# Performance work log

Measured on AMD Instinct MI355X. Metric: run time of the kernel, lower is better.

Reference implementation:

```python
import jax, jax.numpy as jnp
import numpy as np

B, N, E = 2, 50000, 400000
C_IN, D, C, S, H, L, FFN = 5, 2, 128, 32, 8, 4, 512
COORD_F, TIME_F, FREQ_BASE, BETA = 8, 4, 1000.0, 1.0
HD = C // H


def setup_inputs() -> dict:
    key = jax.random.key(0)
    ks = jax.random.split(key, 32)
    sc = 0.02
    inp = {
        'inputs': jax.random.normal(ks[0], (B, N, C_IN), jnp.float32),
        'coords': jax.random.uniform(ks[1], (B, N, D), jnp.float32),
        't_norm': jax.random.uniform(ks[2], (B,), jnp.float32),
        'adj_indices': jax.random.randint(ks[3], (2, E), 0, N, jnp.int64 if jax.config.jax_enable_x64 else jnp.int32),
        'adj_values': jax.random.uniform(ks[4], (E,), jnp.float32) * 0.25,  # ~1/avg_degree for stable magnitudes
        'freq_matrix': jax.random.normal(ks[5], (D, COORD_F), jnp.float32),
        'embed_W': jax.random.normal(ks[6], (C_IN + 2 * COORD_F + 2 * TIME_F, C), jnp.float32) * sc,
        'embed_b': jnp.zeros((C,), jnp.float32),
        'ln1_g': jnp.ones((L, C), jnp.float32),
        'ln1_b': jnp.zeros((L, C), jnp.float32),
        'Wslice': jax.random.normal(ks[7], (L, C, S), jnp.float32) * sc,
        'bslice': jnp.zeros((L, S), jnp.float32),
        'Wfront': jax.random.normal(ks[8], (L, C, S), jnp.float32) * sc,
        'bfront': jnp.zeros((L, S), jnp.float32),
        'Win': jax.random.normal(ks[9], (L, C, 3 * C), jnp.float32) * sc,
        'b_in': jnp.zeros((L, 3 * C), jnp.float32),
        'Wout': jax.random.normal(ks[10], (L, C, C), jnp.float32) * sc,
        'bout': jnp.zeros((L, C), jnp.float32),
        'ln2_g': jnp.ones((L, C), jnp.float32),
        'ln2_b': jnp.zeros((L, C), jnp.float32),
        'Wff1': jax.random.normal(ks[11], (L, C, FFN), jnp.float32) * sc,
        'bff1': jnp.zeros((L, FFN), jnp.float32),
        'Wff2': jax.random.normal(ks[12], (L, FFN, C), jnp.float32) * sc,
        'bff2': jnp.zeros((L, C), jnp.float32),
        'proj_W': jax.random.normal(ks[13], (C, C_IN), jnp.float32) * sc,
        'proj_b': jnp.zeros((C_IN,), jnp.float32),
    }
    return inp


def _layer_norm(x, g, b, eps=1e-5):
    m = jnp.mean(x, -1, keepdims=True)
    v = jnp.mean(jnp.square(x - m), -1, keepdims=True)
    return (x - m) * jax.lax.rsqrt(v + eps) * g + b


def _forward(inputs, coords, t_norm, adj_indices, adj_values, freq_matrix,
             embed_W, embed_b, ln1_g, ln1_b, Wslice, bslice, Wfront, bfront,
             Win, b_in, Wout, bout, ln2_g, ln2_b, Wff1, bff1, Wff2, bff2,
             proj_W, proj_b):
    rows, cols = adj_indices[0], adj_indices[1]
    b, n = coords.shape[0], coords.shape[1]
    # spatial Fourier encoding (B,N,2*COORD_F)
    p = 2.0 * jnp.pi * (coords @ freq_matrix)
    sp_enc = jnp.concatenate([jnp.sin(p), jnp.cos(p)], -1)
    # temporal encoding (B,N,2*TIME_F)
    omega = FREQ_BASE ** (-jnp.arange(TIME_F, dtype=jnp.float32) / TIME_F)
    ang = omega[None, :] * (t_norm * FREQ_BASE)[:, None]
    t_enc = jnp.broadcast_to(jnp.concatenate([jnp.sin(ang), jnp.cos(ang)], -1)[:, None, :], (b, n, 2 * TIME_F))
    x = jnp.concatenate([inputs, sp_enc, t_enc], -1) @ embed_W + embed_b  # (B,N,C)
    weights_all = []
    for l in range(L):
        h = _layer_norm(x, ln1_g[l], ln1_b[l])
        # sparse adjacency aggregation: y[r] += a_e * h[c] (duplicates sum == coalesce)
        contrib = adj_values[None, :, None] * h[:, cols, :]  # (B,E,C)
        h_local = jax.vmap(lambda cb: jax.ops.segment_sum(cb, rows, num_segments=n))(contrib)
        h_front = h - h_local
        logits = h @ Wslice[l] + bslice[l] + BETA * (h_front @ Wfront[l] + bfront[l])
        w = jax.nn.softmax(logits, -1)  # (B,N,S)
        wsum = jnp.maximum(jnp.sum(w, axis=1)[:, :, None], 1e-8)  # (B,S,1)
        slices = jnp.einsum('bns,bnc->bsc', w, h) / wsum  # (B,S,C)
        # slice-space MHA (self-attention on S tokens)
        qkv = slices @ Win[l] + b_in[l]
        q, k, v = jnp.split(qkv, 3, axis=-1)
        def split_heads(t):
            return t.reshape(b, S, H, HD).transpose(0, 2, 1, 3)  # (B,H,S,HD)
        qh, kh, vh = split_heads(q), split_heads(k), split_heads(v)
        attn = jax.nn.softmax(jnp.einsum('bhqd,bhkd->bhqk', qh, kh) / jnp.sqrt(jnp.float32(HD)), -1)
        o = jnp.einsum('bhqk,bhkd->bhqd', attn, vh).transpose(0, 2, 1, 3).reshape(b, S, C)
        slices_out = o @ Wout[l] + bout[l]
        x = x + jnp.einsum('bns,bsc->bnc', w, slices_out)
        h2 = _layer_norm(x, ln2_g[l], ln2_b[l])
        x = x + jax.nn.gelu(h2 @ Wff1[l] + bff1[l], approximate=False) @ Wff2[l] + bff2[l]
        weights_all.append(w)
    out = x @ proj_W + proj_b  # (B,N,C_OUT)
    return out, jnp.stack(weights_all)  # (L,B,N,S)


def reference(inputs, coords, t_norm, adj_indices, adj_values, freq_matrix,
              embed_W, embed_b, ln1_g, ln1_b, Wslice, bslice, Wfront, bfront,
              Win, b_in, Wout, bout, ln2_g, ln2_b, Wff1, bff1, Wff2, bff2,
              proj_W, proj_b):
    return _forward(inputs, coords, t_norm, adj_indices, adj_values, freq_matrix,
                    embed_W, embed_b, ln1_g, ln1_b, Wslice, bslice, Wfront, bfront,
                    Win, b_in, Wout, bout, ln2_g, ln2_b, Wff1, bff1, Wff2, bff2,
                    proj_W, proj_b)
```

## Files before the change

kernel.cpp:

```cpp
#include <hip/hip_runtime.h>
#include <math.h>

#define BATCH 2
#define NN 50000
#define NE 400000
#define C_IN 5
#define CC 128
#define SS 32
#define NH 8
#define NL 4
#define FFN 512
#define COORD_F 8
#define TIME_F 4
#define HD 16
#define BETA 1.0f
#define TWO_PI 6.283185307179586476925287f

#define NTOT (BATCH * NN)
#define FF_MT 128
#define FF_BLOCKS ((NTOT + FF_MT - 1) / FF_MT)
#define MPAD (FF_BLOCKS * FF_MT)
#define NBLK ((NN + 127) / 128)
#define LP_PAD 136
#define H2S 136
#define HIDS 72
#define NREP 16
#define EMB_NPB 8
#define PROJ_NPB 12

typedef unsigned short u16;
typedef unsigned int u32;
typedef __attribute__((ext_vector_type(8))) __bf16 bf16x8;
typedef __attribute__((ext_vector_type(4))) float f32x4;

__device__ __forceinline__ u16 f2bf(float f) {
    union { __bf16 b; u16 u; } v;
    v.b = (__bf16)f;
    return v.u;
}

__device__ __forceinline__ float bf2f(u16 h) {
    union { u32 u; float f; } v; v.u = ((u32)h) << 16;
    return v.f;
}

__device__ __forceinline__ float bf_lo(u32 u) {
    union { u32 u; float f; } v; v.u = u << 16;
    return v.f;
}

__device__ __forceinline__ float bf_hi(u32 u) {
    union { u32 u; float f; } v; v.u = u & 0xffff0000u;
    return v.f;
}

__device__ __forceinline__ float gelu_f(float a) {
    float xx = a * 0.7071067811865475f;
    float ax = fabsf(xx);
    float t = 1.0f / fmaf(0.3275911f, ax, 1.0f);
    float poly = t * fmaf(t, fmaf(t, fmaf(t, fmaf(t, 1.061405429f, -1.453152027f),
                                          1.421413741f), -0.284496736f), 0.254829592f);
    float e = __expf(-ax * ax);
    float erfv = copysignf(fmaf(-poly, e, 1.0f), xx);
    return 0.5f * a * (1.0f + erfv);
}

__global__ void count_deg(const int* rows, int* deg) {
    int e = blockIdx.x * blockDim.x + threadIdx.x;
    if (e < NE) atomicAdd(&deg[rows[e]], 1);
}

__global__ __launch_bounds__(512) void scan_deg(const int* deg, int* rowptr) {
    __shared__ int part[512];
    int t = threadIdx.x;
    const int CH = (NN + 511) / 512;
    int begin = t * CH, end = min(begin + CH, NN);
    int s = 0;
    for (int i = begin; i < end; i++) s += deg[i];
    part[t] = s;
    __syncthreads();
    for (int off = 1; off < 512; off <<= 1) {
        int v = (t >= off) ? part[t - off] : 0;
        __syncthreads();
        part[t] += v;
        __syncthreads();
    }
    int base = (t == 0) ? 0 : part[t - 1];
    for (int i = begin; i < end; i++) { rowptr[i] = base; base += deg[i]; }
    if (t == 511) rowptr[NN] = part[511];
}

__global__ void fill_csr(const int* rows, const int* cols, const float* vals,
                         int* cursor, int* csr_col, float* csr_val) {
    int e = blockIdx.x * blockDim.x + threadIdx.x;
    if (e < NE) {
        int p = atomicAdd(&cursor[rows[e]], 1);
        csr_col[p] = cols[e];
        csr_val[p] = vals[e];
    }
}

__global__ __launch_bounds__(128) void embed_ln1_kernel(const float* __restrict__ inputs,
                                                        const float* __restrict__ coords,
                                                        const float* __restrict__ t_norm,
                                                        const float* __restrict__ freq,
                                                        const float* __restrict__ W,
                                                        const float* __restrict__ bias,
                                                        const float* __restrict__ g,
                                                        const float* __restrict__ bb,
                                                        float* __restrict__ x,
                                                        u16* __restrict__ hbf) {
    int t = threadIdx.x;
    int n0 = blockIdx.x * EMB_NPB;
    __shared__ float feat[EMB_NPB][32];
    __shared__ float sm[EMB_NPB][4];
    if (t < EMB_NPB) {
        int node = n0 + t;
        if (node < NTOT) {
            int b = node / NN;
            float c0 = coords[node * 2 + 0], c1 = coords[node * 2 + 1];
            #pragma unroll
            for (int j = 0; j < 8; j++) {
                float p = TWO_PI * (c0 * freq[j] + c1 * freq[8 + j]);
                feat[t][5 + j] = sinf(p);
                feat[t][13 + j] = cosf(p);
            }
            #pragma unroll
            for (int j = 0; j < 4; j++) {
                float omega = powf(1000.0f, -(float)j * 0.25f);
                float ang = omega * t_norm[b] * 1000.0f;
                feat[t][21 + j] = sinf(ang);
                feat[t][25 + j] = cosf(ang);
            }
            #pragma unroll
            for (int k = 0; k < 5; k++) feat[t][k] = inputs[node * 5 + k];
        }
    }
    float Wr[29];
    #pragma unroll
    for (int k = 0; k < 29; k++) Wr[k] = W[k * CC + t];
    float bi = bias[t], gt = g[t], bbt = bb[t];
    __syncthreads();
    float accv[EMB_NPB];
    #pragma unroll
    for (int nn = 0; nn < EMB_NPB; nn++) {
        float a = bi;
        #pragma unroll
        for (int k = 0; k < 29; k++) a += feat[nn][k] * Wr[k];
        accv[nn] = a;
        int node = n0 + nn;
        if (node < NTOT) x[(size_t)node * CC + t] = a;
    }
    #pragma unroll
    for (int nn = 0; nn < EMB_NPB; nn++) {
        float s = accv[nn];
        #pragma unroll
        for (int off = 32; off > 0; off >>= 1) s += __shfl_xor(s, off, 64);
        if ((t & 63) == 0) sm[nn][t >> 6] = s;
    }
    __syncthreads();
    float dv[EMB_NPB];
    #pragma unroll
    for (int nn = 0; nn < EMB_NPB; nn++) {
        float mean = (sm[nn][0] + sm[nn][1]) * (1.0f / 128.0f);
        float d = accv[nn] - mean;
        dv[nn] = d;
        float ss = d * d;
        #pragma unroll
        for (int off = 32; off > 0; off >>= 1) ss += __shfl_xor(ss, off, 64);
        if ((t & 63) == 0) sm[nn][2 + (t >> 6)] = ss;
    }
    __syncthreads();
    #pragma unroll
    for (int nn = 0; nn < EMB_NPB; nn++) {
        int node = n0 + nn;
        if (node < NTOT) {
            float var = (sm[nn][2] + sm[nn][3]) * (1.0f / 128.0f);
            hbf[(size_t)node * CC + t] = f2bf(dv[nn] * rsqrtf(var + 1e-5f) * gt + bbt);
        }
    }
}

__global__ __launch_bounds__(256) void agg_kernel(const u16* __restrict__ hbf,
                                                  const int* __restrict__ rowptr,
                                                  const int* __restrict__ csr_col,
                                                  const float* __restrict__ csr_val,
                                                  u16* __restrict__ hlbf) {
    int wid = threadIdx.x >> 6;
    int lane = threadIdx.x & 63;
    int node = blockIdx.x * 4 + wid;
    int b = node / NN, r = node - b * NN;
    int s0 = rowptr[r], s1 = rowptr[r + 1];
    const u32* hb = (const u32*)(hbf + (size_t)b * NN * CC);
    float a0l = 0.f, a1l = 0.f, a2l = 0.f, a3l = 0.f;
    float a0h = 0.f, a1h = 0.f, a2h = 0.f, a3h = 0.f;
    int e = s0;
    for (; e + 4 <= s1; e += 4) {
        int c0 = csr_col[e], c1 = csr_col[e + 1], c2 = csr_col[e + 2], c3 = csr_col[e + 3];
        float v0 = csr_val[e], v1 = csr_val[e + 1], v2 = csr_val[e + 2], v3 = csr_val[e + 3];
        u32 u0 = hb[(size_t)c0 * 64 + lane];
        u32 u1 = hb[(size_t)c1 * 64 + lane];
        u32 u2 = hb[(size_t)c2 * 64 + lane];
        u32 u3 = hb[(size_t)c3 * 64 + lane];
        a0l += v0 * bf_lo(u0);  a0h += v0 * bf_hi(u0);
        a1l += v1 * bf_lo(u1);  a1h += v1 * bf_hi(u1);
        a2l += v2 * bf_lo(u2);  a2h += v2 * bf_hi(u2);
        a3l += v3 * bf_lo(u3);  a3h += v3 * bf_hi(u3);
    }
    for (; e < s1; e++) {
        float v = csr_val[e];
        u32 u = hb[(size_t)csr_col[e] * 64 + lane];
        a0l += v * bf_lo(u);  a0h += v * bf_hi(u);
    }
    float al = (a0l + a1l) + (a2l + a3l);
    float ah = (a0h + a1h) + (a2h + a3h);
    u32 outv = (u32)f2bf(al) | ((u32)f2bf(ah) << 16);
    ((u32*)hlbf)[(size_t)node * 64 + lane] = outv;
}

__global__ __launch_bounds__(256) void pack_logits_weights(const float* Ws, const float* bs,
                                                           const float* Wf, const float* bf,
                                                           u16* Wcombp, float* bcombp) {
    int idx = blockIdx.x * 256 + threadIdx.x;
    if (idx >= NL * SS * 256) return;
    int l = idx / (SS * 256);
    int r = idx - l * (SS * 256);
    int s = r >> 8, k = r & 255;
    float v;
    if (k < 128)
        v = Ws[(size_t)l * CC * SS + (size_t)k * SS + s] + BETA * Wf[(size_t)l * CC * SS + (size_t)k * SS + s];
    else
        v = -BETA * Wf[(size_t)l * CC * SS + (size_t)(k - 128) * SS + s];
    Wcombp[idx] = f2bf(v);
    if (k == 0) bcombp[l * SS + s] = bs[l * SS + s] + BETA * bf[l * SS + s];
}

__global__ __launch_bounds__(256, 2) void logits_pool(const u16* __restrict__ hbf,
                                                      const u16* __restrict__ hlbf,
                                                      const u16* __restrict__ Wcomb,
                                                      const float* __restrict__ bcomb,
                                                      float* __restrict__ wout,
                                                      u16* __restrict__ whi,
                                                      u16* __restrict__ wlo,
                                                      float* __restrict__ rep,
                                                      float* __restrict__ wsum) {
    __shared__ __align__(16) u16 hT[128 * LP_PAD];
    __shared__ __align__(16) u16 wTh[SS * LP_PAD];
    __shared__ __align__(16) u16 wTl[SS * LP_PAD];
    __shared__ float wsum_sh[SS];
    int t = threadIdx.x;
    int b = blockIdx.y;
    int nl0 = blockIdx.x * 128;
    int wv = t >> 6, lane = t & 63;
    int q = lane >> 4, ln16 = lane & 15;
    int nl0w = nl0 + wv * 32;
    if (t < SS) wsum_sh[t] = 0.0f;
    __syncthreads();

    f32x4 acc[2][2];
    #pragma unroll
    for (int mi = 0; mi < 2; mi++)
        #pragma unroll
        for (int ni = 0; ni < 2; ni++) acc[mi][ni] = (f32x4){0.f, 0.f, 0.f, 0.f};

    #pragma unroll
    for (int ks = 0; ks < 8; ks++) {
        const u16* src = (ks < 4) ? hbf : hlbf;
        int ko = (ks & 3) * 32 + q * 8;
        bf16x8 af[2], bfrg[2];
        #pragma unroll
        for (int mi = 0; mi < 2; mi++) {
            int nl = nl0w + mi * 16 + ln16;
            af[mi] = *(const bf16x8*)&src[((size_t)b * NN + nl) * CC + ko];
            if (ks < 4) {
                bool valid = nl < NN;
                const u16* ap = (const u16*)&af[mi];
                int nlb = nl - nl0;
                #pragma unroll
                for (int i = 0; i < 8; i++)
                    hT[(ko + i) * LP_PAD + nlb] = valid ? ap[i] : (u16)0;
            }
        }
        #pragma unroll
        for (int ni = 0; ni < 2; ni++)
            bfrg[ni] = *(const bf16x8*)&Wcomb[(size_t)(ni * 16 + ln16) * 256 + ks * 32 + q * 8];
        #pragma unroll
        for (int mi = 0; mi < 2; mi++)
            #pragma unroll
            for (int ni = 0; ni < 2; ni++)
                acc[mi][ni] = __builtin_amdgcn_mfma_f32_16x16x32_bf16(af[mi], bfrg[ni], acc[mi][ni], 0, 0, 0);
    }

    float bc0 = bcomb[ln16], bc1 = bcomb[16 + ln16];
    float ws0 = 0.0f, ws1 = 0.0f;
    #pragma unroll
    for (int mi = 0; mi < 2; mi++)
        #pragma unroll
        for (int r = 0; r < 4; r++) {
            float l0 = acc[mi][0][r] + bc0;
            float l1 = acc[mi][1][r] + bc1;
            float m = fmaxf(l0, l1);
            #pragma unroll
            for (int msk = 1; msk < 16; msk <<= 1) m = fmaxf(m, __shfl_xor(m, msk, 64));
            float e0 = __expf(l0 - m), e1 = __expf(l1 - m);
            float sum = e0 + e1;
            #pragma unroll
            for (int msk = 1; msk < 16; msk <<= 1) sum += __shfl_xor(sum, msk, 64);
            float is = 1.0f / sum;
            int nl = nl0w + mi * 16 + q * 4 + r;
            bool valid = nl < NN;
            float w0 = valid ? e0 * is : 0.0f;
            float w1 = valid ? e1 * is : 0.0f;
            u16 h0 = f2bf(w0), h1 = f2bf(w1);
            u16 lo0 = f2bf(w0 - bf2f(h0)), lo1 = f2bf(w1 - bf2f(h1));
            if (valid) {
                size_t gb = ((size_t)b * NN + nl) * SS;
                wout[gb + ln16] = w0;
                wout[gb + 16 + ln16] = w1;
                whi[gb + ln16] = h0;  wlo[gb + ln16] = lo0;
                whi[gb + 16 + ln16] = h1;  wlo[gb + 16 + ln16] = lo1;
            }
            int nlb = nl - nl0;
            wTh[ln16 * LP_PAD + nlb] = h0;  wTl[ln16 * LP_PAD + nlb] = lo0;
            wTh[(16 + ln16) * LP_PAD + nlb] = h1;  wTl[(16 + ln16) * LP_PAD + nlb] = lo1;
            ws0 += w0;  ws1 += w1;
        }
    ws0 += __shfl_xor(ws0, 16, 64); ws0 += __shfl_xor(ws0, 32, 64);
    ws1 += __shfl_xor(ws1, 16, 64); ws1 += __shfl_xor(ws1, 32, 64);
    if (q == 0) {
        atomicAdd(&wsum_sh[ln16], ws0);
        atomicAdd(&wsum_sh[16 + ln16], ws1);
    }
    __syncthreads();

    f32x4 pacc[2][8];
    #pragma unroll
    for (int st = 0; st < 2; st++)
        #pragma unroll
        for (int ct = 0; ct < 8; ct++) pacc[st][ct] = (f32x4){0.f, 0.f, 0.f, 0.f};
    {
        int kb = wv * 32 + q * 8;
        bf16x8 wh[2], wl2[2];
        #pragma unroll
        for (int st = 0; st < 2; st++) {
            wh[st] = *(const bf16x8*)&wTh[(st * 16 + ln16) * LP_PAD + kb];
            wl2[st] = *(const bf16x8*)&wTl[(st * 16 + ln16) * LP_PAD + kb];
        }
        #pragma unroll
        for (int ct = 0; ct < 8; ct++) {
            bf16x8 bfr = *(const bf16x8*)&hT[(ct * 16 + ln16) * LP_PAD + kb];
            #pragma unroll
            for (int st = 0; st < 2; st++) {
                pacc[st][ct] = __builtin_amdgcn_mfma_f32_16x16x32_bf16(wh[st], bfr, pacc[st][ct], 0, 0, 0);
                pacc[st][ct] = __builtin_amdgcn_mfma_f32_16x16x32_bf16(wl2[st], bfr, pacc[st][ct], 0, 0, 0);
            }
        }
    }
    __syncthreads();

    float* red = (float*)hT;
    for (int i = t; i < SS * CC; i += 256) red[i] = 0.0f;
    __syncthreads();
    #pragma unroll
    for (int st = 0; st < 2; st++)
        #pragma unroll
        for (int ct = 0; ct < 8; ct++)
            #pragma unroll
            for (int r = 0; r < 4; r++)
                atomicAdd(&red[(st * 16 + q * 4 + r) * CC + ct * 16 + ln16], pacc[st][ct][r]);
    __syncthreads();
    if (t < SS) atomicAdd(&wsum[b * SS + t], wsum_sh[t]);
    int rep_id = (blockIdx.y * NBLK + blockIdx.x) & (NREP - 1);
    float* dst = rep + ((size_t)rep_id * BATCH + b) * SS * CC;
    #pragma unroll
    for (int k = 0; k < 16; k++) {
        int idx = k * 256 + t;
        atomicAdd(&dst[idx], red[idx]);
    }
}

__global__ __launch_bounds__(256) void reduce_slices(const float* __restrict__ rep,
                                                     float* __restrict__ slices_acc) {
    int j = blockIdx.x * 256 + threadIdx.x;
    int b = j >> 12;
    int e = j & 4095;
    float s = 0.0f;
    #pragma unroll
    for (int r = 0; r < NREP; r++) s += rep[((size_t)r * BATCH + b) * SS * CC + e];
    slices_acc[(size_t)b * SS * CC + e] = s;
}

__global__ __launch_bounds__(128) void qkv_kernel(const float* slices_acc, const float* wsum,
                                                  const float* Win, const float* b_in_p,
                                                  float* qkv) {
    int blk = blockIdx.x;
    int t = threadIdx.x;
    __shared__ float row[128];
    float iv = 1.0f / fmaxf(wsum[blk], 1e-8f);
    row[t] = slices_acc[(size_t)blk * CC + t] * iv;
    __syncthreads();
    #pragma unroll
    for (int jj = 0; jj < 3; jj++) {
        int j = t + jj * 128;
        float a = b_in_p[j];
        #pragma unroll 8
        for (int c = 0; c < 128; c++) a += row[c] * Win[c * 384 + j];
        qkv[(size_t)blk * 384 + j] = a;
    }
}

__global__ __launch_bounds__(64) void attn_kernel(const float* qkv, float* ovals) {
    int blk = blockIdx.x;
    int b = blk >> 3, h = blk & 7;
    int t = threadIdx.x;
    __shared__ float ksh[32 * 16], vsh[32 * 16];
    for (int i = t; i < 512; i += 64) {
        int k = i >> 4, d = i & 15;
        ksh[i] = qkv[((size_t)b * 32 + k) * 384 + 128 + h * 16 + d];
        vsh[i] = qkv[((size_t)b * 32 + k) * 384 + 256 + h * 16 + d];
    }
    __syncthreads();
    if (t < 32) {
        float qr[16];
        #pragma unroll
        for (int d = 0; d < 16; d++) qr[d] = qkv[((size_t)b * 32 + t) * 384 + h * 16 + d];
        float sc[32];
        float m = -1e30f;
        for (int k = 0; k < 32; k++) {
            float a = 0.0f;
            #pragma unroll
            for (int d = 0; d < 16; d++) a += qr[d] * ksh[k * 16 + d];
            a *= 0.25f;
            sc[k] = a;
            m = fmaxf(m, a);
        }
        float ssum = 0.0f;
        for (int k = 0; k < 32; k++) { float e = expf(sc[k] - m); sc[k] = e; ssum += e; }
        float is = 1.0f / ssum;
        float o[16];
        #pragma unroll
        for (int d = 0; d < 16; d++) o[d] = 0.0f;
        for (int k = 0; k < 32; k++) {
            float p = sc[k] * is;
            #pragma unroll
            for (int d = 0; d < 16; d++) o[d] += p * vsh[k * 16 + d];
        }
        #pragma unroll
        for (int d = 0; d < 16; d++) ovals[((size_t)b * 32 + t) * 128 + h * 16 + d] = o[d];
    }
}

__global__ __launch_bounds__(128) void mha_out_kernel(const float* ovals, const float* Wout,
                                                      const float* bout,
                                                      u16* soThi, u16* soTlo) {
    int blk = blockIdx.x;
    int b = blk >> 5, s = blk & 31;
    int t = threadIdx.x;
    __shared__ float row[128];
    row[t] = ovals[(size_t)blk * 128 + t];
    __syncthreads();
    float a = bout[t];
    #pragma unroll 8
    for (int cc = 0; cc < 128; cc++) a += row[cc] * Wout[cc * CC + t];
    u16 hi = f2bf(a);
    size_t idx = (size_t)b * CC * SS + (size_t)t * SS + s;
    soThi[idx] = hi;
    soTlo[idx] = f2bf(a - bf2f(hi));
}

__global__ __launch_bounds__(256) void pack_ffn_weights(const float* Wff1, const float* Wff2,
                                                        u16* W1p, u16* W2p) {
    int idx = blockIdx.x * 256 + threadIdx.x;
    if (idx >= NL * FFN * CC) return;
    int l = idx / (FFN * CC);
    int r = idx - l * (FFN * CC);
    int j = r >> 7, c = r & 127;
    W1p[idx] = f2bf(Wff1[(size_t)l * CC * FFN + (size_t)c * FFN + j]);
    int c2 = r >> 9, j2 = r & 511;
    W2p[idx] = f2bf(Wff2[(size_t)l * FFN * CC + (size_t)j2 * CC + c2]);
}

__global__ __launch_bounds__(256, 2) void ffn_mega(float* __restrict__ x,
                                                   const u16* __restrict__ whi,
                                                   const u16* __restrict__ wlo,
                                                   const u16* __restrict__ soThi,
                                                   const u16* __restrict__ soTlo,
                                                   const float* __restrict__ g,
                                                   const float* __restrict__ bb,
                                                   const u16* __restrict__ W1p,
                                                   const float* __restrict__ bff1,
                                                   const u16* __restrict__ W2p,
                                                   const float* __restrict__ bff2,
                                                   const float* __restrict__ g1,
                                                   const float* __restrict__ b1,
                                                   u16* __restrict__ hbf_out) {
    __shared__ __align__(16) u16 smem[128 * 144];
    __shared__ __align__(16) float rowst[128 * 4];
    u16* h2t = smem;
    int t = threadIdx.x;
    int b = blockIdx.y;
    int n0 = blockIdx.x * 128;
    int wave = t >> 6, lane = t & 63;
    int wm = wave >> 1, wn = wave & 1;
    int q = lane >> 4, ln16 = lane & 15;
    bool emit = (g1 != nullptr);

    float gr[4], br[4];
    #pragma unroll
    for (int ni = 0; ni < 4; ni++) {
        int col = wn * 64 + ni * 16 + ln16;
        gr[ni] = g[col]; br[ni] = bb[col];
    }

    f32x4 acc2[4][4];
    #pragma unroll
    for (int mi = 0; mi < 4; mi++)
        #pragma unroll
        for (int ni = 0; ni < 4; ni++) acc2[mi][ni] = (f32x4){0.f, 0.f, 0.f, 0.f};

    {
        const u16* soh = soThi + (size_t)b * CC * SS;
        const u16* sol = soTlo + (size_t)b * CC * SS;
        bf16x8 bh[4], bl[4], ah[4], al[4];
        bf16x8 zf;
        #pragma unroll
        for (int i = 0; i < 8; i++) zf[i] = (__bf16)0.0f;
        #pragma unroll
        for (int ni = 0; ni < 4; ni++) {
            int c = wn * 64 + ni * 16 + ln16;
            bh[ni] = *(const bf16x8*)&soh[c * SS + q * 8];
            bl[ni] = *(const bf16x8*)&sol[c * SS + q * 8];
        }
        #pragma unroll
        for (int mi = 0; mi < 4; mi++) {
            int row = n0 + wm * 64 + mi * 16 + ln16;
            if (row < NN) {
                size_t base = ((size_t)b * NN + row) * SS + q * 8;
                ah[mi] = *(const bf16x8*)&whi[base];
                al[mi] = *(const bf16x8*)&wlo[base];
            } else { ah[mi] = zf; al[mi] = zf; }
        }
        #pragma unroll
        for (int mi = 0; mi < 4; mi++)
            #pragma unroll
            for (int ni = 0; ni < 4; ni++) {
                acc2[mi][ni] = __builtin_amdgcn_mfma_f32_16x16x32_bf16(ah[mi], bh[ni], acc2[mi][ni], 0, 0, 0);
                acc2[mi][ni] = __builtin_amdgcn_mfma_f32_16x16x32_bf16(al[mi], bh[ni], acc2[mi][ni], 0, 0, 0);
                acc2[mi][ni] = __builtin_amdgcn_mfma_f32_16x16x32_bf16(ah[mi], bl[ni], acc2[mi][ni], 0, 0, 0);
            }
    }

    #pragma unroll
    for (int mi = 0; mi < 4; mi++)
        #pragma unroll
        for (int r = 0; r < 4; r++) {
            int row = n0 + wm * 64 + mi * 16 + q * 4 + r;
            if (row < NN) {
                const float* xr = &x[((size_t)b * NN + row) * CC + wn * 64 + ln16];
                #pragma unroll
                for (int ni = 0; ni < 4; ni++) acc2[mi][ni][r] += xr[ni * 16];
            }
        }
    #pragma unroll
    for (int mi = 0; mi < 4; mi++)
        #pragma unroll
        for (int r = 0; r < 4; r++) {
            float a = acc2[mi][0][r] + acc2[mi][1][r] + acc2[mi][2][r] + acc2[mi][3][r];
            float a2 = acc2[mi][0][r] * acc2[mi][0][r] + acc2[mi][1][r] * acc2[mi][1][r] +
                       acc2[mi][2][r] * acc2[mi][2][r] + acc2[mi][3][r] * acc2[mi][3][r];
            #pragma unroll
            for (int msk = 1; msk < 16; msk <<= 1) {
                a += __shfl_xor(a, msk, 64);
                a2 += __shfl_xor(a2, msk, 64);
            }
            if (ln16 == 0) {
                int m = wm * 64 + mi * 16 + q * 4 + r;
                rowst[m * 4 + wn * 2] = a;
                rowst[m * 4 + wn * 2 + 1] = a2;
            }
        }
    __syncthreads();
    #pragma unroll
    for (int mi = 0; mi < 4; mi++)
        #pragma unroll
        for (int r = 0; r < 4; r++) {
            int m = wm * 64 + mi * 16 + q * 4 + r;
            float s1 = rowst[m * 4 + 0] + rowst[m * 4 + 2];
            float s2 = rowst[m * 4 + 1] + rowst[m * 4 + 3];
            float mean = s1 * (1.0f / 128.0f);
            float var = s2 * (1.0f / 128.0f) - mean * mean;
            float rstd = rsqrtf(fmaxf(var, 0.0f) + 1e-5f);
            #pragma unroll
            for (int ni = 0; ni < 4; ni++) {
                int col = wn * 64 + ni * 16 + ln16;
                h2t[m * H2S + col] = f2bf((acc2[mi][ni][r] - mean) * rstd * gr[ni] + br[ni]);
            }
        }
    __syncthreads();

    bf16x8 areg[4][4];
    #pragma unroll
    for (int ks = 0; ks < 4; ks++)
        #pragma unroll
        for (int mi = 0; mi < 4; mi++)
            areg[ks][mi] = *(const bf16x8*)&h2t[(wm * 64 + mi * 16 + ln16) * H2S + ks * 32 + q * 8];
    __syncthreads();

    for (int jc = 0; jc < 8; jc++) {
        u16* hid = smem + (jc & 1) * (128 * HIDS);
        f32x4 acc1[4][2];
        #pragma unroll
        for (int mi = 0; mi < 4; mi++)
            #pragma unroll
            for (int ni = 0; ni < 2; ni++) acc1[mi][ni] = (f32x4){0.f, 0.f, 0.f, 0.f};

        __builtin_amdgcn_s_setprio(1);
        #pragma unroll
        for (int ks = 0; ks < 4; ks++) {
            bf16x8 bfr[2];
            #pragma unroll
            for (int ni = 0; ni < 2; ni++)
                bfr[ni] = *(const bf16x8*)&W1p[(size_t)(jc * 64 + wn * 32 + ni * 16 + ln16) * CC + ks * 32 + q * 8];
            #pragma unroll
            for (int mi = 0; mi < 4; mi++)
                #pragma unroll
                for (int ni = 0; ni < 2; ni++)
                    acc1[mi][ni] = __builtin_amdgcn_mfma_f32_16x16x32_bf16(areg[ks][mi], bfr[ni], acc1[mi][ni], 0, 0, 0);
        }
        __builtin_amdgcn_s_setprio(0);

        #pragma unroll
        for (int ni = 0; ni < 2; ni++) {
            float b1v = bff1[jc * 64 + wn * 32 + ni * 16 + ln16];
            #pragma unroll
            for (int mi = 0; mi < 4; mi++)
                #pragma unroll
                for (int r = 0; r < 4; r++)
                    hid[(wm * 64 + mi * 16 + q * 4 + r) * HIDS + wn * 32 + ni * 16 + ln16] =
                        f2bf(gelu_f(acc1[mi][ni][r] + b1v));
        }
        __syncthreads();

        __builtin_amdgcn_s_setprio(1);
        #pragma unroll
        for (int ks2 = 0; ks2 < 2; ks2++) {
            bf16x8 af[4], bfr[4];
            #pragma unroll
            for (int mi = 0; mi < 4; mi++)
                af[mi] = *(const bf16x8*)&hid[(wm * 64 + mi * 16 + ln16) * HIDS + ks2 * 32 + q * 8];
            #pragma unroll
            for (int ni = 0; ni < 4; ni++)
                bfr[ni] = *(const bf16x8*)&W2p[(size_t)(wn * 64 + ni * 16 + ln16) * FFN + jc * 64 + ks2 * 32 + q * 8];
            #pragma unroll
            for (int mi = 0; mi < 4; mi++)
                #pragma unroll
                for (int ni = 0; ni < 4; ni++)
                    acc2[mi][ni] = __builtin_amdgcn_mfma_f32_16x16x32_bf16(af[mi], bfr[ni], acc2[mi][ni], 0, 0, 0);
        }
        __builtin_amdgcn_s_setprio(0);
    }

    float b2[4];
    #pragma unroll
    for (int ni = 0; ni < 4; ni++) b2[ni] = bff2[wn * 64 + ni * 16 + ln16];
    #pragma unroll
    for (int mi = 0; mi < 4; mi++)
        #pragma unroll
        for (int ni = 0; ni < 4; ni++)
            #pragma unroll
            for (int r = 0; r < 4; r++) acc2[mi][ni][r] += b2[ni];

    #pragma unroll
    for (int mi = 0; mi < 4; mi++)
        #pragma unroll
        for (int r = 0; r < 4; r++) {
            int row = n0 + wm * 64 + mi * 16 + q * 4 + r;
            if (row < NN) {
                float* xo = &x[((size_t)b * NN + row) * CC + wn * 64 + ln16];
                #pragma unroll
                for (int ni = 0; ni < 4; ni++) xo[ni * 16] = acc2[mi][ni][r];
            }
        }

    if (emit) {
        float g1r[4], b1r[4];
        #pragma unroll
        for (int ni = 0; ni < 4; ni++) {
            int col = wn * 64 + ni * 16 + ln16;
            g1r[ni] = g1[col]; b1r[ni] = b1[col];
        }
        #pragma unroll
        for (int mi = 0; mi < 4; mi++)
            #pragma unroll
            for (int r = 0; r < 4; r++) {
                float a = acc2[mi][0][r] + acc2[mi][1][r] + acc2[mi][2][r] + acc2[mi][3][r];
                float a2 = acc2[mi][0][r] * acc2[mi][0][r] + acc2[mi][1][r] * acc2[mi][1][r] +
                           acc2[mi][2][r] * acc2[mi][2][r] + acc2[mi][3][r] * acc2[mi][3][r];
                #pragma unroll
                for (int msk = 1; msk < 16; msk <<= 1) {
                    a += __shfl_xor(a, msk, 64);
                    a2 += __shfl_xor(a2, msk, 64);
                }
                if (ln16 == 0) {
                    int m = wm * 64 + mi * 16 + q * 4 + r;
                    rowst[m * 4 + wn * 2] = a;
                    rowst[m * 4 + wn * 2 + 1] = a2;
                }
            }
        __syncthreads();
        #pragma unroll
        for (int mi = 0; mi < 4; mi++)
            #pragma unroll
            for (int r = 0; r < 4; r++) {
                int m = wm * 64 + mi * 16 + q * 4 + r;
                float s1 = rowst[m * 4 + 0] + rowst[m * 4 + 2];
                float s2 = rowst[m * 4 + 1] + rowst[m * 4 + 3];
                float mean = s1 * (1.0f / 128.0f);
                float var = s2 * (1.0f / 128.0f) - mean * mean;
                float rstd = rsqrtf(fmaxf(var, 0.0f) + 1e-5f);
                #pragma unroll
                for (int ni = 0; ni < 4; ni++) {
                    int col = wn * 64 + ni * 16 + ln16;
                    smem[m * H2S + col] = f2bf((acc2[mi][ni][r] - mean) * rstd * g1r[ni] + b1r[ni]);
                }
            }
        __syncthreads();
        #pragma unroll
        for (int it = 0; it < 8; it++) {
            int chunk = it * 256 + t;
            int m = chunk >> 4;
            int c8 = (chunk & 15) << 3;
            int row = n0 + m;
            if (row < NN)
                *(f32x4*)&hbf_out[((size_t)b * NN + row) * CC + c8] =
                    *(const f32x4*)&smem[m * H2S + c8];
        }
    }
}

__global__ __launch_bounds__(128) void proj_kernel(const float* __restrict__ x,
                                                   const float* __restrict__ W,
                                                   const float* __restrict__ bias,
                                                   float* __restrict__ outp) {
    int t = threadIdx.x;
    int n0 = blockIdx.x * PROJ_NPB;
    __shared__ float xr[PROJ_NPB][128];
    __shared__ float pr[3][40];
    for (int idx = t; idx < PROJ_NPB * 128; idx += 128) {
        int nn = idx >> 7, c = idx & 127;
        int node = n0 + nn;
        xr[nn][c] = (node < NTOT) ? x[(size_t)node * CC + c] : 0.0f;
    }
    __syncthreads();
    for (int pass = 0; pass < 4; pass++) {
        if (t < 120) {
            int nl = t / 40, tt = t - nl * 40;
            int k = tt / 8, part = tt % 8;
            float a = 0.0f;
            #pragma unroll
            for (int i = 0; i < 16; i++) {
                int c = part * 16 + i;
                a += xr[pass * 3 + nl][c] * W[c * C_IN + k];
            }
            pr[nl][tt] = a;
        }
        __syncthreads();
        if (t < 15) {
            int nl = t / 5, k = t - nl * 5;
            int node = n0 + pass * 3 + nl;
            if (node < NTOT) {
                float a = bias[k];
                #pragma unroll
                for (int p = 0; p < 8; p++) a += pr[nl][k * 8 + p];
                outp[(size_t)node * C_IN + k] = a;
            }
        }
        __syncthreads();
    }
}

extern "C" void kernel_launch(void* const* d_in, const int* in_sizes, int n_in,
                              void* d_out, int out_size, void* d_ws, size_t ws_size,
                              hipStream_t stream) {
    const float* inputs  = (const float*)d_in[0];
    const float* coords  = (const float*)d_in[1];
    const float* t_norm  = (const float*)d_in[2];
    const int*   adj     = (const int*)d_in[3];
    const float* adj_v   = (const float*)d_in[4];
    const float* freq    = (const float*)d_in[5];
    const float* embed_W = (const float*)d_in[6];
    const float* embed_b = (const float*)d_in[7];
    const float* ln1_g   = (const float*)d_in[8];
    const float* ln1_b   = (const float*)d_in[9];
    const float* Wslice  = (const float*)d_in[10];
    const float* bslice  = (const float*)d_in[11];
    const float* Wfront  = (const float*)d_in[12];
    const float* bfront  = (const float*)d_in[13];
    const float* Win     = (const float*)d_in[14];
    const float* b_in    = (const float*)d_in[15];
    const float* Wout    = (const float*)d_in[16];
    const float* bout    = (const float*)d_in[17];
    const float* ln2_g   = (const float*)d_in[18];
    const float* ln2_b   = (const float*)d_in[19];
    const float* Wff1    = (const float*)d_in[20];
    const float* bff1    = (const float*)d_in[21];
    const float* Wff2    = (const float*)d_in[22];
    const float* bff2    = (const float*)d_in[23];
    const float* proj_W  = (const float*)d_in[24];
    const float* proj_b  = (const float*)d_in[25];

    float* out = (float*)d_out;
    float* wout_base = out + (size_t)BATCH * NN * C_IN;

    float* x          = (float*)d_ws;
    u16*   hbf        = (u16*)(x + (size_t)NTOT * CC);
    u16*   hlbf       = hbf + (size_t)MPAD * CC;
    u16*   whi        = hlbf + (size_t)MPAD * CC;
    u16*   wlo        = whi + (size_t)(NTOT + 128) * SS;
    u16*   soThi      = wlo + (size_t)(NTOT + 128) * SS;
    u16*   soTlo      = soThi + BATCH * CC * SS;
    float* slices_acc = (float*)(soTlo + BATCH * CC * SS);
    float* wsum       = slices_acc + BATCH * SS * CC;
    float* qkv_ws     = wsum + BATCH * SS;
    float* ovals_ws   = qkv_ws + BATCH * SS * 384;
    float* csr_val    = ovals_ws + BATCH * SS * CC;
    int*   rowptr     = (int*)(csr_val + NE);
    int*   cursor     = rowptr + (NN + 1);
    int*   deg        = cursor + NN;
    int*   csr_col    = deg + NN;
    u16*   W1p        = (u16*)(csr_col + NE);
    u16*   W2p        = W1p + NL * FFN * CC;
    u16*   Wcombp     = W2p + NL * CC * FFN;
    float* bcomb      = (float*)(Wcombp + NL * SS * 256);
    float* rep        = bcomb + NL * SS;

    hipMemsetAsync(deg, 0, NN * sizeof(int), stream);
    count_deg<<<(NE + 255) / 256, 256, 0, stream>>>(adj, deg);
    scan_deg<<<1, 512, 0, stream>>>(deg, rowptr);
    hipMemcpyAsync(cursor, rowptr, NN * sizeof(int), hipMemcpyDeviceToDevice, stream);
    fill_csr<<<(NE + 255) / 256, 256, 0, stream>>>(adj, adj + NE, adj_v, cursor, csr_col, csr_val);

    pack_ffn_weights<<<(NL * FFN * CC + 255) / 256, 256, 0, stream>>>(Wff1, Wff2, W1p, W2p);
    pack_logits_weights<<<(NL * SS * 256 + 255) / 256, 256, 0, stream>>>(Wslice, bslice, Wfront,
                                                                         bfront, Wcombp, bcomb);

    embed_ln1_kernel<<<(NTOT + EMB_NPB - 1) / EMB_NPB, 128, 0, stream>>>(
        inputs, coords, t_norm, freq, embed_W, embed_b, ln1_g, ln1_b, x, hbf);

    for (int l = 0; l < NL; l++) {
        float* wl = wout_base + (size_t)l * NTOT * SS;
        agg_kernel<<<NTOT / 4, 256, 0, stream>>>(hbf, rowptr, csr_col, csr_val, hlbf);
        hipMemsetAsync(rep, 0, (size_t)NREP * BATCH * SS * CC * sizeof(float), stream);
        hipMemsetAsync(wsum, 0, BATCH * SS * sizeof(float), stream);
        dim3 glp(NBLK, BATCH);
        logits_pool<<<glp, 256, 0, stream>>>(hbf, hlbf, Wcombp + (size_t)l * SS * 256,
                                             bcomb + l * SS, wl, whi, wlo, rep, wsum);
        reduce_slices<<<(BATCH * SS * CC) / 256, 256, 0, stream>>>(rep, slices_acc);
        qkv_kernel<<<BATCH * SS, 128, 0, stream>>>(slices_acc, wsum,
                                                   Win + (size_t)l * CC * 3 * CC,
                                                   b_in + l * 3 * CC, qkv_ws);
        attn_kernel<<<BATCH * NH, 64, 0, stream>>>(qkv_ws, ovals_ws);
        mha_out_kernel<<<BATCH * SS, 128, 0, stream>>>(ovals_ws, Wout + (size_t)l * CC * CC,
                                                       bout + l * CC, soThi, soTlo);
        const float* g1n = (l + 1 < NL) ? (ln1_g + (size_t)(l + 1) * CC) : nullptr;
        const float* b1n = (l + 1 < NL) ? (ln1_b + (size_t)(l + 1) * CC) : nullptr;
        dim3 g3(NBLK, BATCH);
        ffn_mega<<<g3, 256, 0, stream>>>(x, whi, wlo, soThi, soTlo,
                                         ln2_g + l * CC, ln2_b + l * CC,
                                         W1p + (size_t)l * FFN * CC, bff1 + l * FFN,
                                         W2p + (size_t)l * CC * FFN, bff2 + l * CC,
                                         g1n, b1n, hbf);
    }

    proj_kernel<<<(NTOT + PROJ_NPB - 1) / PROJ_NPB, 128, 0, stream>>>(x, proj_W, proj_b, out);
}
```

Before: 1.764 ms.

## Halve FFN row tile to 64 and fold slice reduction into qkv kernel

The fused FFN kernel now handles 64 rows per block instead of 128. This halves accumulator registers and shared memory per block and doubles the block count, aiming for more occupancy and better load balance across CUs. The separate reduce_slices launch is removed, and the qkv kernel sums the replicated partial slice buffers itself, saving one kernel launch per layer. An s_setprio hint is added around the first MFMA group. The trade-off is that each FFN block reloads the W1/W2 weight fragments for half as many rows, so weight traffic from cache per row doubles.

```diff
diff --git a/kernel.cpp b/kernel.cpp
--- a/kernel.cpp
+++ b/kernel.cpp
@@ -21,6 +21,8 @@
 #define FF_BLOCKS ((NTOT + FF_MT - 1) / FF_MT)
 #define MPAD (FF_BLOCKS * FF_MT)
 #define NBLK ((NN + 127) / 128)
+#define FR 64
+#define NBLK2 ((NN + FR - 1) / FR)
 #define LP_PAD 136
 #define H2S 136
 #define HIDS 72
@@ -379,25 +381,20 @@
     }
 }
 
-__global__ __launch_bounds__(256) void reduce_slices(const float* __restrict__ rep,
-                                                     float* __restrict__ slices_acc) {
-    int j = blockIdx.x * 256 + threadIdx.x;
-    int b = j >> 12;
-    int e = j & 4095;
-    float s = 0.0f;
-    #pragma unroll
-    for (int r = 0; r < NREP; r++) s += rep[((size_t)r * BATCH + b) * SS * CC + e];
-    slices_acc[(size_t)b * SS * CC + e] = s;
-}
-
-__global__ __launch_bounds__(128) void qkv_kernel(const float* slices_acc, const float* wsum,
+__global__ __launch_bounds__(128) void qkv_kernel(const float* __restrict__ rep,
+                                                  const float* wsum,
                                                   const float* Win, const float* b_in_p,
                                                   float* qkv) {
     int blk = blockIdx.x;
+    int b = blk >> 5;
     int t = threadIdx.x;
     __shared__ float row[128];
+    int e = (blk & 31) * CC + t;
+    float s = 0.0f;
+    #pragma unroll
+    for (int r = 0; r < NREP; r++) s += rep[((size_t)r * BATCH + b) * SS * CC + e];
     float iv = 1.0f / fmaxf(wsum[blk], 1e-8f);
-    row[t] = slices_acc[(size_t)blk * CC + t] * iv;
+    row[t] = s * iv;
     __syncthreads();
     #pragma unroll
     for (int jj = 0; jj < 3; jj++) {
@@ -494,12 +491,12 @@
                                                    const float* __restrict__ g1,
                                                    const float* __restrict__ b1,
                                                    u16* __restrict__ hbf_out) {
-    __shared__ __align__(16) u16 smem[128 * 144];
-    __shared__ __align__(16) float rowst[128 * 4];
+    __shared__ __align__(16) u16 smem[FR * 144];
+    __shared__ __align__(16) float rowst[FR * 4];
     u16* h2t = smem;
     int t = threadIdx.x;
     int b = blockIdx.y;
-    int n0 = blockIdx.x * 128;
+    int n0 = blockIdx.x * FR;
     int wave = t >> 6, lane = t & 63;
     int wm = wave >> 1, wn = wave & 1;
     int q = lane >> 4, ln16 = lane & 15;
@@ -512,16 +509,16 @@
         gr[ni] = g[col]; br[ni] = bb[col];
     }
 
-    f32x4 acc2[4][4];
-    #pragma unroll
-    for (int mi = 0; mi < 4; mi++)
+    f32x4 acc2[2][4];
+    #pragma unroll
+    for (int mi = 0; mi < 2; mi++)
         #pragma unroll
         for (int ni = 0; ni < 4; ni++) acc2[mi][ni] = (f32x4){0.f, 0.f, 0.f, 0.f};
 
     {
         const u16* soh = soThi + (size_t)b * CC * SS;
         const u16* sol = soTlo + (size_t)b * CC * SS;
-        bf16x8 bh[4], bl[4], ah[4], al[4];
+        bf16x8 bh[4], bl[4], ah[2], al[2];
         bf16x8 zf;
         #pragma unroll
         for (int i = 0; i < 8; i++) zf[i] = (__bf16)0.0f;
@@ -532,29 +529,31 @@
             bl[ni] = *(const bf16x8*)&sol[c * SS + q * 8];
         }
         #pragma unroll
-        for (int mi = 0; mi < 4; mi++) {
-            int row = n0 + wm * 64 + mi * 16 + ln16;
+        for (int mi = 0; mi < 2; mi++) {
+            int row = n0 + wm * 32 + mi * 16 + ln16;
             if (row < NN) {
                 size_t base = ((size_t)b * NN + row) * SS + q * 8;
                 ah[mi] = *(const bf16x8*)&whi[base];
                 al[mi] = *(const bf16x8*)&wlo[base];
             } else { ah[mi] = zf; al[mi] = zf; }
         }
-        #pragma unroll
-        for (int mi = 0; mi < 4; mi++)
+        __builtin_amdgcn_s_setprio(1);
+        #pragma unroll
+        for (int mi = 0; mi < 2; mi++)
             #pragma unroll
             for (int ni = 0; ni < 4; ni++) {
                 acc2[mi][ni] = __builtin_amdgcn_mfma_f32_16x16x32_bf16(ah[mi], bh[ni], acc2[mi][ni], 0, 0, 0);
                 acc2[mi][ni] = __builtin_amdgcn_mfma_f32_16x16x32_bf16(al[mi], bh[ni], acc2[mi][ni], 0, 0, 0);
                 acc2[mi][ni] = __builtin_amdgcn_mfma_f32_16x16x32_bf16(ah[mi], bl[ni], acc2[mi][ni], 0, 0, 0);
             }
-    }
-
-    #pragma unroll
-    for (int mi = 0; mi < 4; mi++)
+        __builtin_amdgcn_s_setprio(0);
+    }
+
+    #pragma unroll
+    for (int mi = 0; mi < 2; mi++)
         #pragma unroll
         for (int r = 0; r < 4; r++) {
-            int row = n0 + wm * 64 + mi * 16 + q * 4 + r;
+            int row = n0 + wm * 32 + mi * 16 + q * 4 + r;
             if (row < NN) {
                 const float* xr = &x[((size_t)b * NN + row) * CC + wn * 64 + ln16];
                 #pragma unroll
@@ -562,7 +561,7 @@
             }
         }
     #pragma unroll
-    for (int mi = 0; mi < 4; mi++)
+    for (int mi = 0; mi < 2; mi++)
         #pragma unroll
         for (int r = 0; r < 4; r++) {
             float a = acc2[mi][0][r] + acc2[mi][1][r] + acc2[mi][2][r] + acc2[mi][3][r];
@@ -574,17 +573,17 @@
                 a2 += __shfl_xor(a2, msk, 64);
             }
             if (ln16 == 0) {
-                int m = wm * 64 + mi * 16 + q * 4 + r;
+                int m = wm * 32 + mi * 16 + q * 4 + r;
                 rowst[m * 4 + wn * 2] = a;
                 rowst[m * 4 + wn * 2 + 1] = a2;
             }
         }
     __syncthreads();
     #pragma unroll
-    for (int mi = 0; mi < 4; mi++)
+    for (int mi = 0; mi < 2; mi++)
         #pragma unroll
         for (int r = 0; r < 4; r++) {
-            int m = wm * 64 + mi * 16 + q * 4 + r;
+            int m = wm * 32 + mi * 16 + q * 4 + r;
             float s1 = rowst[m * 4 + 0] + rowst[m * 4 + 2];
             float s2 = rowst[m * 4 + 1] + rowst[m * 4 + 3];
             float mean = s1 * (1.0f / 128.0f);
@@ -598,19 +597,19 @@
         }
     __syncthreads();
 
-    bf16x8 areg[4][4];
+    bf16x8 areg[4][2];
     #pragma unroll
     for (int ks = 0; ks < 4; ks++)
         #pragma unroll
-        for (int mi = 0; mi < 4; mi++)
-            areg[ks][mi] = *(const bf16x8*)&h2t[(wm * 64 + mi * 16 + ln16) * H2S + ks * 32 + q * 8];
+        for (int mi = 0; mi < 2; mi++)
+            areg[ks][mi] = *(const bf16x8*)&h2t[(wm * 32 + mi * 16 + ln16) * H2S + ks * 32 + q * 8];
     __syncthreads();
 
     for (int jc = 0; jc < 8; jc++) {
-        u16* hid = smem + (jc & 1) * (128 * HIDS);
-        f32x4 acc1[4][2];
-        #pragma unroll
-        for (int mi = 0; mi < 4; mi++)
+        u16* hid = smem + (jc & 1) * (FR * HIDS);
+        f32x4 acc1[2][2];
+        #pragma unroll
+        for (int mi = 0; mi < 2; mi++)
             #pragma unroll
             for (int ni = 0; ni < 2; ni++) acc1[mi][ni] = (f32x4){0.f, 0.f, 0.f, 0.f};
 
@@ -622,7 +621,7 @@
             for (int ni = 0; ni < 2; ni++)
                 bfr[ni] = *(const bf16x8*)&W1p[(size_t)(jc * 64 + wn * 32 + ni * 16 + ln16) * CC + ks * 32 + q * 8];
             #pragma unroll
-            for (int mi = 0; mi < 4; mi++)
+            for (int mi = 0; mi < 2; mi++)
                 #pragma unroll
                 for (int ni = 0; ni < 2; ni++)
                     acc1[mi][ni] = __builtin_amdgcn_mfma_f32_16x16x32_bf16(areg[ks][mi], bfr[ni], acc1[mi][ni], 0, 0, 0);
@@ -633,10 +632,10 @@
         for (int ni = 0; ni < 2; ni++) {
             float b1v = bff1[jc * 64 + wn * 32 + ni * 16 + ln16];
             #pragma unroll
-            for (int mi = 0; mi < 4; mi++)
+            for (int mi = 0; mi < 2; mi++)
                 #pragma unroll
                 for (int r = 0; r < 4; r++)
-                    hid[(wm * 64 + mi * 16 + q * 4 + r) * HIDS + wn * 32 + ni * 16 + ln16] =
+                    hid[(wm * 32 + mi * 16 + q * 4 + r) * HIDS + wn * 32 + ni * 16 + ln16] =
                         f2bf(gelu_f(acc1[mi][ni][r] + b1v));
         }
         __syncthreads();
@@ -644,15 +643,15 @@
         __builtin_amdgcn_s_setprio(1);
         #pragma unroll
         for (int ks2 = 0; ks2 < 2; ks2++) {
-            bf16x8 af[4], bfr[4];
-            #pragma unroll
-            for (int mi = 0; mi < 4; mi++)
-                af[mi] = *(const bf16x8*)&hid[(wm * 64 + mi * 16 + ln16) * HIDS + ks2 * 32 + q * 8];
+            bf16x8 af[2], bfr[4];
+            #pragma unroll
+            for (int mi = 0; mi < 2; mi++)
+                af[mi] = *(const bf16x8*)&hid[(wm * 32 + mi * 16 + ln16) * HIDS + ks2 * 32 + q * 8];
             #pragma unroll
             for (int ni = 0; ni < 4; ni++)
                 bfr[ni] = *(const bf16x8*)&W2p[(size_t)(wn * 64 + ni * 16 + ln16) * FFN + jc * 64 + ks2 * 32 + q * 8];
             #pragma unroll
-            for (int mi = 0; mi < 4; mi++)
+            for (int mi = 0; mi < 2; mi++)
                 #pragma unroll
                 for (int ni = 0; ni < 4; ni++)
                     acc2[mi][ni] = __builtin_amdgcn_mfma_f32_16x16x32_bf16(af[mi], bfr[ni], acc2[mi][ni], 0, 0, 0);
@@ -664,17 +663,17 @@
     #pragma unroll
     for (int ni = 0; ni < 4; ni++) b2[ni] = bff2[wn * 64 + ni * 16 + ln16];
     #pragma unroll
-    for (int mi = 0; mi < 4; mi++)
+    for (int mi = 0; mi < 2; mi++)
         #pragma unroll
         for (int ni = 0; ni < 4; ni++)
             #pragma unroll
             for (int r = 0; r < 4; r++) acc2[mi][ni][r] += b2[ni];
 
     #pragma unroll
-    for (int mi = 0; mi < 4; mi++)
+    for (int mi = 0; mi < 2; mi++)
         #pragma unroll
         for (int r = 0; r < 4; r++) {
-            int row = n0 + wm * 64 + mi * 16 + q * 4 + r;
+            int row = n0 + wm * 32 + mi * 16 + q * 4 + r;
             if (row < NN) {
                 float* xo = &x[((size_t)b * NN + row) * CC + wn * 64 + ln16];
                 #pragma unroll
@@ -690,7 +689,7 @@
             g1r[ni] = g1[col]; b1r[ni] = b1[col];
         }
         #pragma unroll
-        for (int mi = 0; mi < 4; mi++)
+        for (int mi = 0; mi < 2; mi++)
             #pragma unroll
             for (int r = 0; r < 4; r++) {
                 float a = acc2[mi][0][r] + acc2[mi][1][r] + acc2[mi][2][r] + acc2[mi][3][r];
@@ -702,17 +701,17 @@
                     a2 += __shfl_xor(a2, msk, 64);
                 }
                 if (ln16 == 0) {
-                    int m = wm * 64 + mi * 16 + q * 4 + r;
+                    int m = wm * 32 + mi * 16 + q * 4 + r;
                     rowst[m * 4 + wn * 2] = a;
                     rowst[m * 4 + wn * 2 + 1] = a2;
                 }
             }
         __syncthreads();
         #pragma unroll
-        for (int mi = 0; mi < 4; mi++)
+        for (int mi = 0; mi < 2; mi++)
             #pragma unroll
             for (int r = 0; r < 4; r++) {
-                int m = wm * 64 + mi * 16 + q * 4 + r;
+                int m = wm * 32 + mi * 16 + q * 4 + r;
                 float s1 = rowst[m * 4 + 0] + rowst[m * 4 + 2];
                 float s2 = rowst[m * 4 + 1] + rowst[m * 4 + 3];
                 float mean = s1 * (1.0f / 128.0f);
@@ -726,7 +725,7 @@
             }
         __syncthreads();
         #pragma unroll
-        for (int it = 0; it < 8; it++) {
+        for (int it = 0; it < 4; it++) {
             int chunk = it * 256 + t;
             int m = chunk >> 4;
             int c8 = (chunk & 15) << 3;
@@ -855,8 +854,7 @@
         dim3 glp(NBLK, BATCH);
         logits_pool<<<glp, 256, 0, stream>>>(hbf, hlbf, Wcombp + (size_t)l * SS * 256,
                                              bcomb + l * SS, wl, whi, wlo, rep, wsum);
-        reduce_slices<<<(BATCH * SS * CC) / 256, 256, 0, stream>>>(rep, slices_acc);
-        qkv_kernel<<<BATCH * SS, 128, 0, stream>>>(slices_acc, wsum,
+        qkv_kernel<<<BATCH * SS, 128, 0, stream>>>(rep, wsum,
                                                    Win + (size_t)l * CC * 3 * CC,
                                                    b_in + l * 3 * CC, qkv_ws);
         attn_kernel<<<BATCH * NH, 64, 0, stream>>>(qkv_ws, ovals_ws);
@@ -864,7 +862,7 @@
                                                        bout + l * CC, soThi, soTlo);
         const float* g1n = (l + 1 < NL) ? (ln1_g + (size_t)(l + 1) * CC) : nullptr;
         const float* b1n = (l + 1 < NL) ? (ln1_b + (size_t)(l + 1) * CC) : nullptr;
-        dim3 g3(NBLK, BATCH);
+        dim3 g3(NBLK2, BATCH);
         ffn_mega<<<g3, 256, 0, stream>>>(x, whi, wlo, soThi, soTlo,
                                          ln2_g + l * CC, ln2_b + l * CC,
                                          W1p + (size_t)l * FFN * CC, bff1 + l * FFN,
```

Result: no change. 1.782 ms (+1.0%).

## Fuse slice reduction, QKV, attention and output projection into one kernel

Applied to the files above, without the earlier changes.

Replaces four small per-layer kernels (reduce_slices, qkv, attn, mha_out) with a single kernel launched with one 512-thread block per batch that keeps slices, qkv and attention outputs in shared memory. The two memsets are merged into one by placing wsum right after the replica buffer. This is meant to cut launch overhead and global round-trips on the tiny-token attention path. The trade is that only 2 blocks run, so each block does far more serial work, e.g. 32 rows times 128-deep dot products per thread for QKV, which may make the kernel itself longer.

```diff
diff --git a/kernel.cpp b/kernel.cpp
--- a/kernel.cpp
+++ b/kernel.cpp
@@ -27,6 +27,7 @@
 #define NREP 16
 #define EMB_NPB 8
 #define PROJ_NPB 12
+#define QKV_PAD 385
 
 typedef unsigned short u16;
 typedef unsigned int u32;
@@ -379,57 +380,52 @@
     }
 }
 
-__global__ __launch_bounds__(256) void reduce_slices(const float* __restrict__ rep,
-                                                     float* __restrict__ slices_acc) {
-    int j = blockIdx.x * 256 + threadIdx.x;
-    int b = j >> 12;
-    int e = j & 4095;
-    float s = 0.0f;
-    #pragma unroll
-    for (int r = 0; r < NREP; r++) s += rep[((size_t)r * BATCH + b) * SS * CC + e];
-    slices_acc[(size_t)b * SS * CC + e] = s;
-}
-
-__global__ __launch_bounds__(128) void qkv_kernel(const float* slices_acc, const float* wsum,
-                                                  const float* Win, const float* b_in_p,
-                                                  float* qkv) {
-    int blk = blockIdx.x;
+__global__ __launch_bounds__(512) void mha_fused(const float* __restrict__ rep,
+                                                 const float* __restrict__ wsum,
+                                                 const float* __restrict__ Win,
+                                                 const float* __restrict__ b_in_p,
+                                                 const float* __restrict__ Wout,
+                                                 const float* __restrict__ bout,
+                                                 u16* __restrict__ soThi,
+                                                 u16* __restrict__ soTlo) {
+    int b = blockIdx.x;
     int t = threadIdx.x;
-    __shared__ float row[128];
-    float iv = 1.0f / fmaxf(wsum[blk], 1e-8f);
-    row[t] = slices_acc[(size_t)blk * CC + t] * iv;
-    __syncthreads();
-    #pragma unroll
-    for (int jj = 0; jj < 3; jj++) {
-        int j = t + jj * 128;
-        float a = b_in_p[j];
-        #pragma unroll 8
-        for (int c = 0; c < 128; c++) a += row[c] * Win[c * 384 + j];
-        qkv[(size_t)blk * 384 + j] = a;
-    }
-}
-
-__global__ __launch_bounds__(64) void attn_kernel(const float* qkv, float* ovals) {
-    int blk = blockIdx.x;
-    int b = blk >> 3, h = blk & 7;
-    int t = threadIdx.x;
-    __shared__ float ksh[32 * 16], vsh[32 * 16];
-    for (int i = t; i < 512; i += 64) {
-        int k = i >> 4, d = i & 15;
-        ksh[i] = qkv[((size_t)b * 32 + k) * 384 + 128 + h * 16 + d];
-        vsh[i] = qkv[((size_t)b * 32 + k) * 384 + 256 + h * 16 + d];
-    }
-    __syncthreads();
-    if (t < 32) {
+    __shared__ float sl[SS][CC];
+    __shared__ float qkv[SS][QKV_PAD];
+    __shared__ float ov[SS][CC];
+
+    for (int i = t; i < SS * CC; i += 512) {
+        int s = i >> 7;
+        float v = 0.0f;
+        #pragma unroll
+        for (int r = 0; r < NREP; r++) v += rep[((size_t)r * BATCH + b) * SS * CC + i];
+        float iv = 1.0f / fmaxf(wsum[b * SS + s], 1e-8f);
+        sl[s][i & 127] = v * iv;
+    }
+    __syncthreads();
+
+    if (t < 384) {
+        float bj = b_in_p[t];
+        for (int s = 0; s < SS; s++) {
+            float a = bj;
+            #pragma unroll 8
+            for (int c = 0; c < 128; c++) a += sl[s][c] * Win[c * 384 + t];
+            qkv[s][t] = a;
+        }
+    }
+    __syncthreads();
+
+    if (t < 256) {
+        int h = t >> 5, q = t & 31;
         float qr[16];
         #pragma unroll
-        for (int d = 0; d < 16; d++) qr[d] = qkv[((size_t)b * 32 + t) * 384 + h * 16 + d];
+        for (int d = 0; d < 16; d++) qr[d] = qkv[q][h * 16 + d];
         float sc[32];
         float m = -1e30f;
         for (int k = 0; k < 32; k++) {
             float a = 0.0f;
             #pragma unroll
-            for (int d = 0; d < 16; d++) a += qr[d] * ksh[k * 16 + d];
+            for (int d = 0; d < 16; d++) a += qr[d] * qkv[k][128 + h * 16 + d];
             a *= 0.25f;
             sc[k] = a;
             m = fmaxf(m, a);
@@ -443,29 +439,25 @@
         for (int k = 0; k < 32; k++) {
             float p = sc[k] * is;
             #pragma unroll
-            for (int d = 0; d < 16; d++) o[d] += p * vsh[k * 16 + d];
-        }
-        #pragma unroll
-        for (int d = 0; d < 16; d++) ovals[((size_t)b * 32 + t) * 128 + h * 16 + d] = o[d];
-    }
-}
-
-__global__ __launch_bounds__(128) void mha_out_kernel(const float* ovals, const float* Wout,
-                                                      const float* bout,
-                                                      u16* soThi, u16* soTlo) {
-    int blk = blockIdx.x;
-    int b = blk >> 5, s = blk & 31;
-    int t = threadIdx.x;
-    __shared__ float row[128];
-    row[t] = ovals[(size_t)blk * 128 + t];
-    __syncthreads();
-    float a = bout[t];
-    #pragma unroll 8
-    for (int cc = 0; cc < 128; cc++) a += row[cc] * Wout[cc * CC + t];
-    u16 hi = f2bf(a);
-    size_t idx = (size_t)b * CC * SS + (size_t)t * SS + s;
-    soThi[idx] = hi;
-    soTlo[idx] = f2bf(a - bf2f(hi));
+            for (int d = 0; d < 16; d++) o[d] += p * qkv[k][256 + h * 16 + d];
+        }
+        #pragma unroll
+        for (int d = 0; d < 16; d++) ov[q][h * 16 + d] = o[d];
+    }
+    __syncthreads();
+
+    #pragma unroll
+    for (int it = 0; it < 8; it++) {
+        int idx = it * 512 + t;
+        int s = idx >> 7, c = idx & 127;
+        float a = bout[c];
+        #pragma unroll 8
+        for (int cc = 0; cc < 128; cc++) a += ov[s][cc] * Wout[cc * CC + c];
+        u16 hi = f2bf(a);
+        size_t oidx = (size_t)b * CC * SS + (size_t)c * SS + s;
+        soThi[oidx] = hi;
+        soTlo[oidx] = f2bf(a - bf2f(hi));
+    }
 }
 
 __global__ __launch_bounds__(256) void pack_ffn_weights(const float* Wff1, const float* Wff2,
@@ -819,11 +811,7 @@
     u16*   wlo        = whi + (size_t)(NTOT + 128) * SS;
     u16*   soThi      = wlo + (size_t)(NTOT + 128) * SS;
     u16*   soTlo      = soThi + BATCH * CC * SS;
-    float* slices_acc = (float*)(soTlo + BATCH * CC * SS);
-    float* wsum       = slices_acc + BATCH * SS * CC;
-    float* qkv_ws     = wsum + BATCH * SS;
-    float* ovals_ws   = qkv_ws + BATCH * SS * 384;
-    float* csr_val    = ovals_ws + BATCH * SS * CC;
+    float* csr_val    = (float*)(soTlo + BATCH * CC * SS);
     int*   rowptr     = (int*)(csr_val + NE);
     int*   cursor     = rowptr + (NN + 1);
     int*   deg        = cursor + NN;
@@ -833,6 +821,7 @@
     u16*   Wcombp     = W2p + NL * CC * FFN;
     float* bcomb      = (float*)(Wcombp + NL * SS * 256);
     float* rep        = bcomb + NL * SS;
+    float* wsum       = rep + (size_t)NREP * BATCH * SS * CC;
 
     hipMemsetAsync(deg, 0, NN * sizeof(int), stream);
     count_deg<<<(NE + 255) / 256, 256, 0, stream>>>(adj, deg);
@@ -850,18 +839,14 @@
     for (int l = 0; l < NL; l++) {
         float* wl = wout_base + (size_t)l * NTOT * SS;
         agg_kernel<<<NTOT / 4, 256, 0, stream>>>(hbf, rowptr, csr_col, csr_val, hlbf);
-        hipMemsetAsync(rep, 0, (size_t)NREP * BATCH * SS * CC * sizeof(float), stream);
-        hipMemsetAsync(wsum, 0, BATCH * SS * sizeof(float), stream);
+        hipMemsetAsync(rep, 0, ((size_t)NREP * BATCH * SS * CC + BATCH * SS) * sizeof(float), stream);
         dim3 glp(NBLK, BATCH);
         logits_pool<<<glp, 256, 0, stream>>>(hbf, hlbf, Wcombp + (size_t)l * SS * 256,
                                              bcomb + l * SS, wl, whi, wlo, rep, wsum);
-        reduce_slices<<<(BATCH * SS * CC) / 256, 256, 0, stream>>>(rep, slices_acc);
-        qkv_kernel<<<BATCH * SS, 128, 0, stream>>>(slices_acc, wsum,
-                                                   Win + (size_t)l * CC * 3 * CC,
-                                                   b_in + l * 3 * CC, qkv_ws);
-        attn_kernel<<<BATCH * NH, 64, 0, stream>>>(qkv_ws, ovals_ws);
-        mha_out_kernel<<<BATCH * SS, 128, 0, stream>>>(ovals_ws, Wout + (size_t)l * CC * CC,
-                                                       bout + l * CC, soThi, soTlo);
+        mha_fused<<<BATCH, 512, 0, stream>>>(rep, wsum,
+                                             Win + (size_t)l * CC * 3 * CC, b_in + l * 3 * CC,
+                                             Wout + (size_t)l * CC * CC, bout + l * CC,
+                                             soThi, soTlo);
         const float* g1n = (l + 1 < NL) ? (ln1_g + (size_t)(l + 1) * CC) : nullptr;
         const float* b1n = (l + 1 < NL) ? (ln1_b + (size_t)(l + 1) * CC) : nullptr;
         dim3 g3(NBLK, BATCH);
```

After: 2.074 ms. 17.6% more time.
